# Optimization experiments

Measured on AMD Instinct MI355X. Metric: run time of the kernel, lower is better.

## Reference

```python
import jax, jax.numpy as jnp
import numpy as np

DIM = 128
EPS = 1e-5  # torch LayerNorm default


def setup_inputs() -> dict:
    key = jax.random.key(0)
    ks = jax.random.split(key, 8)
    N = 262144
    x = jax.random.normal(ks[0], (N, DIM), dtype=jnp.float32)
    # Parameters (stored as [in, out] for jax matmul); scale ~ torch default init
    ln_w = jnp.ones((DIM,), dtype=jnp.float32)
    ln_b = jnp.zeros((DIM,), dtype=jnp.float32)
    s1 = 1.0 / np.sqrt(DIM)
    s2 = 1.0 / np.sqrt(2 * DIM)
    w1 = jax.random.uniform(ks[1], (DIM, 2 * DIM), jnp.float32, -s1, s1)
    b1 = jax.random.uniform(ks[2], (2 * DIM,), jnp.float32, -s1, s1)
    w2 = jax.random.uniform(ks[3], (2 * DIM, DIM), jnp.float32, -s2, s2)
    b2 = jax.random.uniform(ks[4], (2 * DIM,), jnp.float32, -s2, s2)[:DIM]
    wg = jax.random.uniform(ks[5], (2 * DIM, DIM), jnp.float32, -s2, s2)
    bg = jax.random.uniform(ks[6], (DIM,), jnp.float32, -s2, s2)
    return {"x": x, "ln_w": ln_w, "ln_b": ln_b, "w1": w1, "b1": b1,
            "w2": w2, "b2": b2, "wg": wg, "bg": bg, "passes": 8}


def reference(x, ln_w, ln_b, w1, b1, w2, b2, wg, bg, passes):
    # Split the gate weight so we avoid materializing the concat [state, refined].
    wg_s, wg_r = wg[:DIM], wg[DIM:]

    def step(state, _):
        mu = jnp.mean(state, axis=-1, keepdims=True)
        var = jnp.mean(jnp.square(state - mu), axis=-1, keepdims=True)
        h = (state - mu) * jax.lax.rsqrt(var + EPS) * ln_w + ln_b
        refined = jax.nn.gelu(h @ w1 + b1, approximate=False) @ w2 + b2
        gate = jax.nn.sigmoid(state @ wg_s + refined @ wg_r + bg)
        return state + gate * refined, None

    state, _ = jax.lax.scan(step, x, None, length=passes)
    return state
```

## Files before the change

### kernel.cpp

```cpp
#include <hip/hip_runtime.h>
#include <math.h>

#define DIM 128
#define HID 256
#define MT 64
#define NT 512
#define H_STRIDE 136
#define G_STRIDE 264
#define D_STRIDE 132

typedef __attribute__((ext_vector_type(8))) short bf16x8;
typedef __attribute__((ext_vector_type(4))) float f32x4;
typedef __attribute__((ext_vector_type(4))) unsigned int u32x4;

#define MFMA(a, b, c) __builtin_amdgcn_mfma_f32_16x16x32_bf16((a), (b), (c), 0, 0, 0)

__device__ __forceinline__ unsigned int pack2(float lo, float hi) {
    unsigned int a = __float_as_uint(lo) + 0x8000u;
    unsigned int b = __float_as_uint(hi) + 0x8000u;
    return __builtin_amdgcn_perm(b, a, 0x07060302u);
}
__device__ __forceinline__ unsigned short rb16(float f) {
    return (unsigned short)((__float_as_uint(f) + 0x8000u) >> 16);
}
__device__ __forceinline__ float frcp(float x) { return __builtin_amdgcn_rcpf(x); }
__device__ __forceinline__ float ex2(float x)  { return __builtin_amdgcn_exp2f(x); }
__device__ __forceinline__ float gelu_f(float t) {
    const float u = t * fmaf(t * t, -0.1029436f, -2.3022082f);
    return t * frcp(1.f + ex2(u));
}
__device__ __forceinline__ float sigm(float x) { return frcp(1.f + ex2(-1.442695f * x)); }
__device__ __forceinline__ f32x4 splat4(float v) { f32x4 r = {v, v, v, v}; return r; }

__global__ void w2g_setup(const float* __restrict__ w2, const float* __restrict__ wg,
                          const float* __restrict__ b2, const float* __restrict__ bg,
                          float* __restrict__ w2g)
{
    __shared__ float wr[DIM][DIM + 1];
    const int t = threadIdx.x;
    for (int i = t; i < DIM * DIM; i += 256)
        wr[i >> 7][i & 127] = wg[DIM * DIM + i];
    __syncthreads();
    const int row = blockIdx.x * 32 + (t >> 3);
    const int c0  = (t & 7) * 16;
    float acc[16];
#pragma unroll
    for (int j = 0; j < 16; ++j) acc[j] = 0.f;
    for (int k = 0; k < DIM; ++k) {
        const float a = w2[row * DIM + k];
#pragma unroll
        for (int j = 0; j < 16; ++j) acc[j] = fmaf(a, wr[k][c0 + j], acc[j]);
    }
#pragma unroll
    for (int j = 0; j < 16; ++j) w2g[row * DIM + c0 + j] = acc[j];
    if (blockIdx.x == 0 && t < DIM) {
        float s = bg[t];
        for (int k = 0; k < DIM; ++k) s = fmaf(b2[k], wr[k][t], s);
        w2g[256 * DIM + t] = s;
    }
}

__global__ __launch_bounds__(NT) void trw_kernel(
    const float* __restrict__ x,
    const float* __restrict__ ln_w, const float* __restrict__ ln_b,
    const float* __restrict__ w1, const float* __restrict__ b1,
    const float* __restrict__ w2, const float* __restrict__ b2,
    const float* __restrict__ wg,
    const float* __restrict__ w2g,
    const int* __restrict__ passes_p,
    float* __restrict__ out, int nrows)
{
    __shared__ __align__(16) unsigned short hBuf[MT * H_STRIDE];
    __shared__ __align__(16) unsigned short gBuf[MT * G_STRIDE];
    __shared__ __align__(16) float dBuf[MT * D_STRIDE];
    __shared__ __align__(16) float muB[MT];
    __shared__ __align__(16) float sgB[MT];
    unsigned int* gBuf32 = (unsigned int*)gBuf;

    const int tid = threadIdx.x;
    const int w = tid >> 6, l = tid & 63, q = l >> 4, c16 = l & 15;
    const int r16 = tid >> 4;
    const int hc  = (tid & 15) << 3;
    const int np = passes_p[0];

    const int colA = 32 * w + c16, colB = colA + 16, colG = 16 * w + c16;
    bf16x8 w1f[2][4], wgsf[4];
#pragma unroll
    for (int kk = 0; kk < 4; ++kk) {
        bf16x8 fa, fb, fg;
#pragma unroll
        for (int j = 0; j < 8; ++j) {
            const int k = kk * 32 + q * 8 + j;
            const float lwk = ln_w[k];
            fa[j] = (short)rb16(lwk * w1[k * HID + colA]);
            fb[j] = (short)rb16(lwk * w1[k * HID + colB]);
            fg[j] = (short)rb16(wg[k * DIM + colG]);
        }
        w1f[0][kk] = fa; w1f[1][kk] = fb; wgsf[kk] = fg;
    }
    bf16x8 w2f[8], w2gf[8];
#pragma unroll
    for (int kk = 0; kk < 8; ++kk) {
        bf16x8 f2, fg;
#pragma unroll
        for (int j = 0; j < 8; ++j) {
            const int p  = kk * 32 + q * 8 + j;
            const int p5 = p & 31;
            const int L  = (p & ~31) + ((p5 & 1) << 4) + (p5 >> 1);
            f2[j] = (short)rb16(w2[L * DIM + colG]);
            fg[j] = (short)rb16(w2g[L * DIM + colG]);
        }
        w2f[kk] = f2; w2gf[kk] = fg;
    }
    float b1vA = b1[colA], b1vB = b1[colB], cs1 = 0.f;
    for (int k = 0; k < DIM; ++k) {
        const float lbk = ln_b[k];
        b1vA = fmaf(lbk, w1[k * HID + colA], b1vA);
        b1vB = fmaf(lbk, w1[k * HID + colB], b1vB);
        cs1 += wg[k * DIM + colG];
    }
    const float b2v = b2[colG];
    const float bgv = w2g[256 * DIM + colG];

#define HUB(S, ADD)                                                                     \
    {                                                                                   \
        if (ADD) {                                                                      \
            _Pragma("unroll")                                                           \
            for (int v = 0; v < 2; ++v) {                                               \
                f32x4 d = *(f32x4*)&dBuf[((S)*32 + r16) * D_STRIDE + hc + 4 * v];       \
                _Pragma("unroll")                                                       \
                for (int j = 0; j < 4; ++j) st##S[4 * v + j] += d[j];                   \
            }                                                                           \
        }                                                                               \
        float s1 = 0.f, s2 = 0.f;                                                       \
        _Pragma("unroll")                                                               \
        for (int j = 0; j < 8; ++j) { s1 += st##S[j]; s2 = fmaf(st##S[j], st##S[j], s2); } \
        _Pragma("unroll")                                                               \
        for (int m = 8; m >= 1; m >>= 1) { s1 += __shfl_xor(s1, m); s2 += __shfl_xor(s2, m); } \
        const float mu = s1 * (1.f / DIM);                                              \
        const float ve = fmaf(-mu, mu, s2 * (1.f / DIM)) + 1e-5f;                       \
        const float rs = rsqrtf(ve);                                                    \
        const float sg = ve * rs;                                                       \
        const float mrs = mu * rs;                                                      \
        unsigned int hp[4];                                                             \
        _Pragma("unroll")                                                               \
        for (int j = 0; j < 4; ++j)                                                     \
            hp[j] = pack2(fmaf(st##S[2 * j], rs, -mrs), fmaf(st##S[2 * j + 1], rs, -mrs)); \
        u32x4 hv = {hp[0], hp[1], hp[2], hp[3]};                                        \
        *(u32x4*)&hBuf[((S)*32 + r16) * H_STRIDE + hc] = hv;                            \
        if ((tid & 15) == 0) { muB[(S)*32 + r16] = mu; sgB[(S)*32 + r16] = sg; }        \
    }

#define M1E1(S, GS)                                                                     \
    {                                                                                   \
        f32x4 acc0[2], acc1[2], accg[2];                                                \
        _Pragma("unroll")                                                               \
        for (int rt = 0; rt < 2; ++rt) {                                                \
            acc0[rt] = splat4(b1vA); acc1[rt] = splat4(b1vB); accg[rt] = splat4(0.f);   \
        }                                                                               \
        _Pragma("unroll")                                                               \
        for (int rt = 0; rt < 2; ++rt)                                                  \
            _Pragma("unroll")                                                           \
            for (int kk = 0; kk < 4; ++kk) {                                            \
                bf16x8 a = *(bf16x8*)&hBuf[((S)*32 + rt * 16 + c16) * H_STRIDE + kk * 32 + q * 8]; \
                acc0[rt] = MFMA(a, w1f[0][kk], acc0[rt]);                               \
                acc1[rt] = MFMA(a, w1f[1][kk], acc1[rt]);                               \
                accg[rt] = MFMA(a, wgsf[kk], accg[rt]);                                 \
            }                                                                           \
        _Pragma("unroll")                                                               \
        for (int rt = 0; rt < 2; ++rt) {                                                \
            f32x4 muv = *(f32x4*)&muB[(S)*32 + rt * 16 + q * 4];                        \
            f32x4 sgv = *(f32x4*)&sgB[(S)*32 + rt * 16 + q * 4];                        \
            _Pragma("unroll")                                                           \
            for (int r = 0; r < 4; ++r) {                                               \
                const int row = (S)*32 + rt * 16 + q * 4 + r;                           \
                gBuf32[row * (G_STRIDE / 2) + 16 * w + c16] =                           \
                    pack2(gelu_f(acc0[rt][r]), gelu_f(acc1[rt][r]));                    \
                GS[rt][r] = fmaf(sgv[r], accg[rt][r], muv[r] * cs1);                    \
            }                                                                           \
        }                                                                               \
    }

#define M2E2(S, GS)                                                                     \
    {                                                                                   \
        f32x4 acc2[2], accr[2];                                                         \
        _Pragma("unroll")                                                               \
        for (int rt = 0; rt < 2; ++rt) { acc2[rt] = splat4(b2v); accr[rt] = splat4(bgv); } \
        _Pragma("unroll")                                                               \
        for (int rt = 0; rt < 2; ++rt)                                                  \
            _Pragma("unroll")                                                           \
            for (int kk = 0; kk < 8; ++kk) {                                            \
                bf16x8 a = *(bf16x8*)&gBuf[((S)*32 + rt * 16 + c16) * G_STRIDE + kk * 32 + q * 8]; \
                acc2[rt] = MFMA(a, w2f[kk], acc2[rt]);                                  \
                accr[rt] = MFMA(a, w2gf[kk], accr[rt]);                                 \
            }                                                                           \
        _Pragma("unroll")                                                               \
        for (int rt = 0; rt < 2; ++rt)                                                  \
            _Pragma("unroll")                                                           \
            for (int r = 0; r < 4; ++r) {                                               \
                const int row = (S)*32 + rt * 16 + q * 4 + r;                           \
                const float gate = sigm(GS[rt][r] + accr[rt][r]);                       \
                dBuf[row * D_STRIDE + 16 * w + c16] = gate * acc2[rt][r];               \
            }                                                                           \
    }

#define FIN(S)                                                                          \
    {                                                                                   \
        float* orow = out + (size_t)(tile * MT + (S)*32 + r16) * DIM + hc;              \
        _Pragma("unroll")                                                               \
        for (int v = 0; v < 2; ++v) {                                                   \
            f32x4 d = *(f32x4*)&dBuf[((S)*32 + r16) * D_STRIDE + hc + 4 * v];           \
            f32x4 o;                                                                    \
            _Pragma("unroll")                                                           \
            for (int j = 0; j < 4; ++j) o[j] = st##S[4 * v + j] + d[j];                 \
            *(f32x4*)(orow + 4 * v) = o;                                                \
        }                                                                               \
    }

    const int nTiles = nrows / MT;
    for (int tile = blockIdx.x; tile < nTiles; tile += gridDim.x) {
        float st0[8], st1[8];
        {
            const float* xr0 = x + (size_t)(tile * MT + r16) * DIM + hc;
            const float* xr1 = xr0 + 32 * DIM;
#pragma unroll
            for (int v = 0; v < 2; ++v) {
                f32x4 a0 = *(const f32x4*)(xr0 + 4 * v);
                f32x4 a1 = *(const f32x4*)(xr1 + 4 * v);
#pragma unroll
                for (int j = 0; j < 4; ++j) { st0[4 * v + j] = a0[j]; st1[4 * v + j] = a1[j]; }
            }
        }

        f32x4 gsA[2], gsB[2];

        HUB(1, false)
        __syncthreads();

        for (int p = 0; p < np; ++p) {
            M1E1(1, gsB)
            HUB(0, (p > 0))
            __syncthreads();
            M2E2(1, gsB)
            M1E1(0, gsA)
            __syncthreads();
            if (p < np - 1) {
                HUB(1, true)
            } else {
                FIN(1)
            }
            M2E2(0, gsA)
            __syncthreads();
        }
        FIN(0)
    }
#undef HUB
#undef M1E1
#undef M2E2
#undef FIN
}

extern "C" void kernel_launch(void* const* d_in, const int* in_sizes, int n_in,
                              void* d_out, int out_size, void* d_ws, size_t ws_size,
                              hipStream_t stream) {
    const float* x    = (const float*)d_in[0];
    const float* ln_w = (const float*)d_in[1];
    const float* ln_b = (const float*)d_in[2];
    const float* w1   = (const float*)d_in[3];
    const float* b1   = (const float*)d_in[4];
    const float* w2   = (const float*)d_in[5];
    const float* b2   = (const float*)d_in[6];
    const float* wg   = (const float*)d_in[7];
    const float* bg   = (const float*)d_in[8];
    const int* passes = (const int*)d_in[9];
    float* out = (float*)d_out;
    float* w2g = (float*)d_ws;

    const int nrows = in_sizes[0] / DIM;
    hipLaunchKernelGGL(w2g_setup, dim3(8), dim3(256), 0, stream, w2, wg, b2, bg, w2g);
    hipLaunchKernelGGL(trw_kernel, dim3(1024), dim3(NT), 0, stream,
                       x, ln_w, ln_b, w1, b1, w2, b2, wg, w2g, passes, out, nrows);
}
```

Baseline: 964.8 us.

## Split block into two 512-thread crews specializing in M1 and M2 stages

Doubles the block to 1024 threads and partitions it into two warp-specialized crews. One crew holds W1/Wg_s fragments and runs the first GEMM plus LayerNorm, the other holds W2/W2g fragments and runs the second GEMM and gated residual. State now lives in shared memory instead of registers so both crews can reach it. This frees registers per thread by halving the weight fragments each thread holds, at the cost of extra LDS traffic, more shared memory, and possible imbalance between the crews.

```diff
diff --git a/kernel.cpp b/kernel.cpp
--- a/kernel.cpp
+++ b/kernel.cpp
@@ -4,10 +4,10 @@
 #define DIM 128
 #define HID 256
 #define MT 64
-#define NT 512
+#define NT 1024
 #define H_STRIDE 136
 #define G_STRIDE 264
-#define D_STRIDE 132
+#define S_STRIDE 132
 
 typedef __attribute__((ext_vector_type(8))) short bf16x8;
 typedef __attribute__((ext_vector_type(4))) float f32x4;
@@ -72,192 +72,185 @@
 {
     __shared__ __align__(16) unsigned short hBuf[MT * H_STRIDE];
     __shared__ __align__(16) unsigned short gBuf[MT * G_STRIDE];
-    __shared__ __align__(16) float dBuf[MT * D_STRIDE];
+    __shared__ __align__(16) float gsBuf[MT * S_STRIDE];
+    __shared__ __align__(16) float stBuf[MT * S_STRIDE];
     __shared__ __align__(16) float muB[MT];
     __shared__ __align__(16) float sgB[MT];
     unsigned int* gBuf32 = (unsigned int*)gBuf;
 
     const int tid = threadIdx.x;
-    const int w = tid >> 6, l = tid & 63, q = l >> 4, c16 = l & 15;
-    const int r16 = tid >> 4;
-    const int hc  = (tid & 15) << 3;
+    const bool crewA = (tid < 512);
+    const int ct = tid & 511;
+    const int wv = (tid >> 6) & 7;
+    const int l = tid & 63, q = l >> 4, c16 = l & 15;
+    const int colG = 16 * wv + c16;
     const int np = passes_p[0];
-
-    const int colA = 32 * w + c16, colB = colA + 16, colG = 16 * w + c16;
-    bf16x8 w1f[2][4], wgsf[4];
-#pragma unroll
-    for (int kk = 0; kk < 4; ++kk) {
-        bf16x8 fa, fb, fg;
-#pragma unroll
-        for (int j = 0; j < 8; ++j) {
-            const int k = kk * 32 + q * 8 + j;
-            const float lwk = ln_w[k];
-            fa[j] = (short)rb16(lwk * w1[k * HID + colA]);
-            fb[j] = (short)rb16(lwk * w1[k * HID + colB]);
-            fg[j] = (short)rb16(wg[k * DIM + colG]);
-        }
-        w1f[0][kk] = fa; w1f[1][kk] = fb; wgsf[kk] = fg;
-    }
-    bf16x8 w2f[8], w2gf[8];
-#pragma unroll
-    for (int kk = 0; kk < 8; ++kk) {
-        bf16x8 f2, fg;
-#pragma unroll
-        for (int j = 0; j < 8; ++j) {
-            const int p  = kk * 32 + q * 8 + j;
-            const int p5 = p & 31;
-            const int L  = (p & ~31) + ((p5 & 1) << 4) + (p5 >> 1);
-            f2[j] = (short)rb16(w2[L * DIM + colG]);
-            fg[j] = (short)rb16(w2g[L * DIM + colG]);
-        }
-        w2f[kk] = f2; w2gf[kk] = fg;
-    }
-    float b1vA = b1[colA], b1vB = b1[colB], cs1 = 0.f;
-    for (int k = 0; k < DIM; ++k) {
-        const float lbk = ln_b[k];
-        b1vA = fmaf(lbk, w1[k * HID + colA], b1vA);
-        b1vB = fmaf(lbk, w1[k * HID + colB], b1vB);
-        cs1 += wg[k * DIM + colG];
-    }
-    const float b2v = b2[colG];
-    const float bgv = w2g[256 * DIM + colG];
-
-#define HUB(S, ADD)                                                                     \
-    {                                                                                   \
-        if (ADD) {                                                                      \
-            _Pragma("unroll")                                                           \
-            for (int v = 0; v < 2; ++v) {                                               \
-                f32x4 d = *(f32x4*)&dBuf[((S)*32 + r16) * D_STRIDE + hc + 4 * v];       \
-                _Pragma("unroll")                                                       \
-                for (int j = 0; j < 4; ++j) st##S[4 * v + j] += d[j];                   \
-            }                                                                           \
+    const int nTiles = nrows / MT;
+
+    bf16x8 wf[16];
+    {
+        bf16x8 z;
+#pragma unroll
+        for (int j = 0; j < 8; ++j) z[j] = 0;
+#pragma unroll
+        for (int i = 0; i < 16; ++i) wf[i] = z;
+    }
+    float bias0 = 0.f, bias1 = 0.f, bias2 = 0.f;
+
+    if (crewA) {
+        const int colA = 32 * wv + c16, colB = colA + 16;
+#pragma unroll
+        for (int kk = 0; kk < 4; ++kk) {
+#pragma unroll
+            for (int j = 0; j < 8; ++j) {
+                const int k = kk * 32 + q * 8 + j;
+                const float lwk = ln_w[k];
+                wf[kk][j]     = (short)rb16(lwk * w1[k * HID + colA]);
+                wf[4 + kk][j] = (short)rb16(lwk * w1[k * HID + colB]);
+                wf[8 + kk][j] = (short)rb16(wg[k * DIM + colG]);
+            }
+        }
+        bias0 = b1[colA]; bias1 = b1[colB]; bias2 = 0.f;
+        for (int k = 0; k < DIM; ++k) {
+            const float lbk = ln_b[k];
+            bias0 = fmaf(lbk, w1[k * HID + colA], bias0);
+            bias1 = fmaf(lbk, w1[k * HID + colB], bias1);
+            bias2 += wg[k * DIM + colG];
+        }
+    } else {
+#pragma unroll
+        for (int kk = 0; kk < 8; ++kk) {
+#pragma unroll
+            for (int j = 0; j < 8; ++j) {
+                const int pk = kk * 32 + q * 8 + j;
+                const int p5 = pk & 31;
+                const int L  = (pk & ~31) + ((p5 & 1) << 4) + (p5 >> 1);
+                wf[kk][j]     = (short)rb16(w2[L * DIM + colG]);
+                wf[8 + kk][j] = (short)rb16(w2g[L * DIM + colG]);
+            }
+        }
+        bias0 = b2[colG]; bias1 = w2g[256 * DIM + colG];
+    }
+
+#define LOADX(H)                                                                        \
+    {                                                                                   \
+        const int row = (H) * 32 + (ct >> 4);                                           \
+        const int hc  = (ct & 15) << 3;                                                 \
+        const float* xr = x + (size_t)(tile * MT + row) * DIM + hc;                     \
+        *(f32x4*)&stBuf[row * S_STRIDE + hc]     = *(const f32x4*)(xr);                 \
+        *(f32x4*)&stBuf[row * S_STRIDE + hc + 4] = *(const f32x4*)(xr + 4);             \
+    }
+
+#define FIN(H)                                                                          \
+    {                                                                                   \
+        const int row = (H) * 32 + (ct >> 4);                                           \
+        const int hc  = (ct & 15) << 3;                                                 \
+        float* orow = out + (size_t)(tile * MT + row) * DIM + hc;                       \
+        *(f32x4*)(orow)     = *(f32x4*)&stBuf[row * S_STRIDE + hc];                     \
+        *(f32x4*)(orow + 4) = *(f32x4*)&stBuf[row * S_STRIDE + hc + 4];                 \
+    }
+
+#define HUB(H)                                                                          \
+    {                                                                                   \
+        const int row = (H) * 32 + (ct >> 4);                                           \
+        const int hc  = (ct & 15) << 3;                                                 \
+        f32x4 a0 = *(f32x4*)&stBuf[row * S_STRIDE + hc];                                \
+        f32x4 a1 = *(f32x4*)&stBuf[row * S_STRIDE + hc + 4];                            \
+        float s1 = 0.f, s2 = 0.f;                                                       \
+        _Pragma("unroll")                                                               \
+        for (int j = 0; j < 4; ++j) {                                                   \
+            s1 += a0[j] + a1[j];                                                        \
+            s2 = fmaf(a0[j], a0[j], fmaf(a1[j], a1[j], s2));                            \
         }                                                                               \
-        float s1 = 0.f, s2 = 0.f;                                                       \
-        _Pragma("unroll")                                                               \
-        for (int j = 0; j < 8; ++j) { s1 += st##S[j]; s2 = fmaf(st##S[j], st##S[j], s2); } \
         _Pragma("unroll")                                                               \
         for (int m = 8; m >= 1; m >>= 1) { s1 += __shfl_xor(s1, m); s2 += __shfl_xor(s2, m); } \
         const float mu = s1 * (1.f / DIM);                                              \
         const float ve = fmaf(-mu, mu, s2 * (1.f / DIM)) + 1e-5f;                       \
         const float rs = rsqrtf(ve);                                                    \
-        const float sg = ve * rs;                                                       \
         const float mrs = mu * rs;                                                      \
-        unsigned int hp[4];                                                             \
-        _Pragma("unroll")                                                               \
-        for (int j = 0; j < 4; ++j)                                                     \
-            hp[j] = pack2(fmaf(st##S[2 * j], rs, -mrs), fmaf(st##S[2 * j + 1], rs, -mrs)); \
-        u32x4 hv = {hp[0], hp[1], hp[2], hp[3]};                                        \
-        *(u32x4*)&hBuf[((S)*32 + r16) * H_STRIDE + hc] = hv;                            \
-        if ((tid & 15) == 0) { muB[(S)*32 + r16] = mu; sgB[(S)*32 + r16] = sg; }        \
-    }
-
-#define M1E1(S, GS)                                                                     \
+        u32x4 hv = {pack2(fmaf(a0[0], rs, -mrs), fmaf(a0[1], rs, -mrs)),                \
+                    pack2(fmaf(a0[2], rs, -mrs), fmaf(a0[3], rs, -mrs)),                \
+                    pack2(fmaf(a1[0], rs, -mrs), fmaf(a1[1], rs, -mrs)),                \
+                    pack2(fmaf(a1[2], rs, -mrs), fmaf(a1[3], rs, -mrs))};               \
+        *(u32x4*)&hBuf[row * H_STRIDE + hc] = hv;                                       \
+        if ((ct & 15) == 0) { muB[row] = mu; sgB[row] = ve * rs; }                      \
+    }
+
+#define M1(H)                                                                           \
     {                                                                                   \
         f32x4 acc0[2], acc1[2], accg[2];                                                \
         _Pragma("unroll")                                                               \
         for (int rt = 0; rt < 2; ++rt) {                                                \
-            acc0[rt] = splat4(b1vA); acc1[rt] = splat4(b1vB); accg[rt] = splat4(0.f);   \
+            acc0[rt] = splat4(bias0); acc1[rt] = splat4(bias1); accg[rt] = splat4(0.f); \
         }                                                                               \
         _Pragma("unroll")                                                               \
         for (int rt = 0; rt < 2; ++rt)                                                  \
             _Pragma("unroll")                                                           \
             for (int kk = 0; kk < 4; ++kk) {                                            \
-                bf16x8 a = *(bf16x8*)&hBuf[((S)*32 + rt * 16 + c16) * H_STRIDE + kk * 32 + q * 8]; \
-                acc0[rt] = MFMA(a, w1f[0][kk], acc0[rt]);                               \
-                acc1[rt] = MFMA(a, w1f[1][kk], acc1[rt]);                               \
-                accg[rt] = MFMA(a, wgsf[kk], accg[rt]);                                 \
+                bf16x8 a = *(bf16x8*)&hBuf[((H) * 32 + rt * 16 + c16) * H_STRIDE + kk * 32 + q * 8]; \
+                acc0[rt] = MFMA(a, wf[kk], acc0[rt]);                                   \
+                acc1[rt] = MFMA(a, wf[4 + kk], acc1[rt]);                               \
+                accg[rt] = MFMA(a, wf[8 + kk], accg[rt]);                               \
             }                                                                           \
         _Pragma("unroll")                                                               \
         for (int rt = 0; rt < 2; ++rt) {                                                \
-            f32x4 muv = *(f32x4*)&muB[(S)*32 + rt * 16 + q * 4];                        \
-            f32x4 sgv = *(f32x4*)&sgB[(S)*32 + rt * 16 + q * 4];                        \
+            f32x4 muv = *(f32x4*)&muB[(H) * 32 + rt * 16 + q * 4];                      \
+            f32x4 sgv = *(f32x4*)&sgB[(H) * 32 + rt * 16 + q * 4];                      \
             _Pragma("unroll")                                                           \
             for (int r = 0; r < 4; ++r) {                                               \
-                const int row = (S)*32 + rt * 16 + q * 4 + r;                           \
-                gBuf32[row * (G_STRIDE / 2) + 16 * w + c16] =                           \
+                const int row = (H) * 32 + rt * 16 + q * 4 + r;                         \
+                gBuf32[row * (G_STRIDE / 2) + colG] =                                   \
                     pack2(gelu_f(acc0[rt][r]), gelu_f(acc1[rt][r]));                    \
-                GS[rt][r] = fmaf(sgv[r], accg[rt][r], muv[r] * cs1);                    \
+                gsBuf[row * S_STRIDE + colG] = fmaf(sgv[r], accg[rt][r], muv[r] * bias2); \
             }                                                                           \
         }                                                                               \
     }
 
-#define M2E2(S, GS)                                                                     \
+#define M2(H)                                                                           \
     {                                                                                   \
         f32x4 acc2[2], accr[2];                                                         \
         _Pragma("unroll")                                                               \
-        for (int rt = 0; rt < 2; ++rt) { acc2[rt] = splat4(b2v); accr[rt] = splat4(bgv); } \
+        for (int rt = 0; rt < 2; ++rt) { acc2[rt] = splat4(bias0); accr[rt] = splat4(bias1); } \
         _Pragma("unroll")                                                               \
         for (int rt = 0; rt < 2; ++rt)                                                  \
             _Pragma("unroll")                                                           \
             for (int kk = 0; kk < 8; ++kk) {                                            \
-                bf16x8 a = *(bf16x8*)&gBuf[((S)*32 + rt * 16 + c16) * G_STRIDE + kk * 32 + q * 8]; \
-                acc2[rt] = MFMA(a, w2f[kk], acc2[rt]);                                  \
-                accr[rt] = MFMA(a, w2gf[kk], accr[rt]);                                 \
+                bf16x8 a = *(bf16x8*)&gBuf[((H) * 32 + rt * 16 + c16) * G_STRIDE + kk * 32 + q * 8]; \
+                acc2[rt] = MFMA(a, wf[kk], acc2[rt]);                                   \
+                accr[rt] = MFMA(a, wf[8 + kk], accr[rt]);                               \
             }                                                                           \
         _Pragma("unroll")                                                               \
         for (int rt = 0; rt < 2; ++rt)                                                  \
             _Pragma("unroll")                                                           \
             for (int r = 0; r < 4; ++r) {                                               \
-                const int row = (S)*32 + rt * 16 + q * 4 + r;                           \
-                const float gate = sigm(GS[rt][r] + accr[rt][r]);                       \
-                dBuf[row * D_STRIDE + 16 * w + c16] = gate * acc2[rt][r];               \
-            }                                                                           \
-    }
-
-#define FIN(S)                                                                          \
-    {                                                                                   \
-        float* orow = out + (size_t)(tile * MT + (S)*32 + r16) * DIM + hc;              \
-        _Pragma("unroll")                                                               \
-        for (int v = 0; v < 2; ++v) {                                                   \
-            f32x4 d = *(f32x4*)&dBuf[((S)*32 + r16) * D_STRIDE + hc + 4 * v];           \
-            f32x4 o;                                                                    \
-            _Pragma("unroll")                                                           \
-            for (int j = 0; j < 4; ++j) o[j] = st##S[4 * v + j] + d[j];                 \
-            *(f32x4*)(orow + 4 * v) = o;                                                \
-        }                                                                               \
-    }
-
-    const int nTiles = nrows / MT;
+                const int row = (H) * 32 + rt * 16 + q * 4 + r;                         \
+                const int idx = row * S_STRIDE + colG;                                  \
+                const float gate = sigm(gsBuf[idx] + accr[rt][r]);                      \
+                stBuf[idx] += gate * acc2[rt][r];                                       \
+            }                                                                           \
+    }
+
     for (int tile = blockIdx.x; tile < nTiles; tile += gridDim.x) {
-        float st0[8], st1[8];
-        {
-            const float* xr0 = x + (size_t)(tile * MT + r16) * DIM + hc;
-            const float* xr1 = xr0 + 32 * DIM;
-#pragma unroll
-            for (int v = 0; v < 2; ++v) {
-                f32x4 a0 = *(const f32x4*)(xr0 + 4 * v);
-                f32x4 a1 = *(const f32x4*)(xr1 + 4 * v);
-#pragma unroll
-                for (int j = 0; j < 4; ++j) { st0[4 * v + j] = a0[j]; st1[4 * v + j] = a1[j]; }
-            }
-        }
-
-        f32x4 gsA[2], gsB[2];
-
-        HUB(1, false)
+        if (crewA) { LOADX(0) } else { LOADX(1) }
         __syncthreads();
-
+        if (!crewA) { HUB(1) }
+        __syncthreads();
         for (int p = 0; p < np; ++p) {
-            M1E1(1, gsB)
-            HUB(0, (p > 0))
+            if (crewA) { M1(1) } else { HUB(0) }
             __syncthreads();
-            M2E2(1, gsB)
-            M1E1(0, gsA)
+            if (crewA) { M1(0) } else { M2(1) }
             __syncthreads();
-            if (p < np - 1) {
-                HUB(1, true)
-            } else {
-                FIN(1)
-            }
-            M2E2(0, gsA)
+            if (crewA) { if (p < np - 1) HUB(1) } else { M2(0) }
             __syncthreads();
         }
-        FIN(0)
-    }
+        if (crewA) { FIN(0) } else { FIN(1) }
+        __syncthreads();
+    }
+#undef LOADX
+#undef FIN
 #undef HUB
-#undef M1E1
-#undef M2E2
-#undef FIN
+#undef M1
+#undef M2
 }
 
 extern "C" void kernel_launch(void* const* d_in, const int* in_sizes, int n_in,
```

New measurement: 934.9 us. 1.03x faster.
